# Kernel optimization log

Hardware: AMD Instinct MI355X
Metric: run time of the kernel (lower is better)

## Reference

```python
import jax, jax.numpy as jnp
import numpy as np

# db4 decomposition filters (as in get_wavelet_filters('db4'))
_H0 = jnp.array([0.0322231, -0.01260397, -0.09921954, 0.2978578,
                 0.80373875, 0.49761867, -0.02963553, -0.07576571], dtype=jnp.float32)
_H1 = jnp.array([0.07576571, -0.02963553, -0.49761867, 0.80373875,
                 -0.2978578, -0.09921954, 0.01260397, 0.0322231], dtype=jnp.float32)
LEVEL = 2
IN_CH, OUT_CH, MODES = 64, 64, 32


def subband_conv2d(x, k2d, stride):
    # depthwise (grouped) conv: same 2D filter applied per channel, NHWC
    C = x.shape[-1]
    k = jnp.tile(k2d[:, :, None, None], (1, 1, 1, C)).astype(x.dtype)  # HWIO, I=1
    return jax.lax.conv_general_dilated(
        x, k, (stride, stride), 'SAME',
        dimension_numbers=('NHWC', 'HWIO', 'NHWC'), feature_group_count=C)


def upsample2d(t):
    B, H, W, C = t.shape
    return jnp.zeros((B, 2 * H, 2 * W, C), t.dtype).at[:, ::2, ::2, :].set(t)


def setup_inputs() -> dict:
    key = jax.random.key(0)
    kx, k1, k2, k3, k4 = jax.random.split(key, 5)
    scale = 1.0 / (IN_CH * OUT_CH)
    wshape = (IN_CH, OUT_CH, MODES, MODES)
    return {
        'x': jax.random.normal(kx, (32, 128, 128, IN_CH), dtype=jnp.float32),
        'weights1': scale * jax.random.uniform(k1, wshape, dtype=jnp.float32),
        'weights2': scale * jax.random.uniform(k2, wshape, dtype=jnp.float32),
        'weights3': scale * jax.random.uniform(k3, wshape, dtype=jnp.float32),
        'weights4': scale * jax.random.uniform(k4, wshape, dtype=jnp.float32),
    }


def reference(x, weights1, weights2, weights3, weights4):
    # H=W=128 == size and divisible by 2**LEVEL: pad branch and effective_level
    # adjustment in the original are no-ops.
    h0, h1 = _H0, _H1
    g0, g1 = h0[::-1], h1[::-1]  # reconstruction filters

    # ---- multi-level 2D DWT (depthwise strided convs per subband) ----
    approx = x
    details = []
    for _ in range(LEVEL):
        lh = subband_conv2d(approx, jnp.outer(h0, h1), 2)
        hl = subband_conv2d(approx, jnp.outer(h1, h0), 2)
        hh = subband_conv2d(approx, jnp.outer(h1, h1), 2)
        approx = subband_conv2d(approx, jnp.outer(h0, h0), 2)
        details.append((lh, hl, hh))

    # ---- per-pixel channel mixing on final LL and last-level details ----
    ah, aw = approx.shape[1], approx.shape[2]
    out_ft = jnp.einsum('bhwi,iohw->bhwo', approx, weights1[:, :, :ah, :aw])
    last_lh, last_hl, last_hh = details[-1]
    dh, dw = last_lh.shape[1], last_lh.shape[2]
    out_lh = jnp.einsum('bhwi,iohw->bhwo', last_lh, weights2[:, :, :dh, :dw])
    out_hl = jnp.einsum('bhwi,iohw->bhwo', last_hl, weights3[:, :, :dh, :dw])
    out_hh = jnp.einsum('bhwi,iohw->bhwo', last_hh, weights4[:, :, :dh, :dw])

    # ---- IDWT reconstruction ----
    # Deepest level: all four subbands contribute. Earlier levels: details are
    # zeroed in the original, and conv(zeros)=0, so only the LL path remains.
    res = (subband_conv2d(upsample2d(out_ft), jnp.outer(g0, g0), 1)
           + subband_conv2d(upsample2d(out_lh), jnp.outer(g0, g1), 1)
           + subband_conv2d(upsample2d(out_hl), jnp.outer(g1, g0), 1)
           + subband_conv2d(upsample2d(out_hh), jnp.outer(g1, g1), 1))
    for _ in range(LEVEL - 1):
        res = subband_conv2d(upsample2d(res), jnp.outer(g0, g0), 1)
    return res
```

## Files before the change

### kernel.cpp

```cpp
#include <hip/hip_runtime.h>


__constant__ float c_h0[8] = {0.0322231f, -0.01260397f, -0.09921954f, 0.2978578f,
                              0.80373875f, 0.49761867f, -0.02963553f, -0.07576571f};
__constant__ float c_h1[8] = {0.07576571f, -0.02963553f, -0.49761867f, 0.80373875f,
                              -0.2978578f, -0.09921954f, 0.01260397f, 0.0322231f};
__constant__ float c_g0[8] = {-0.07576571f, -0.02963553f, 0.49761867f, 0.80373875f,
                              0.2978578f, -0.09921954f, -0.01260397f, 0.0322231f};
__constant__ float c_g1[8] = {0.0322231f, 0.01260397f, -0.09921954f, -0.2978578f,
                              0.80373875f, -0.49761867f, -0.02963553f, 0.07576571f};

__device__ __forceinline__ float4 f4z() { return make_float4(0.f, 0.f, 0.f, 0.f); }
__device__ __forceinline__ float4 f4fma(float4 a, float w, float4 v) {
  a.x = fmaf(w, v.x, a.x); a.y = fmaf(w, v.y, a.y);
  a.z = fmaf(w, v.z, a.z); a.w = fmaf(w, v.w, a.w);
  return a;
}

__global__ __launch_bounds__(256) void k_dwt1t(const float* __restrict__ x,
                                               float* __restrict__ ll1,
                                               const float* __restrict__ w1,
                                               const float* __restrict__ w2,
                                               const float* __restrict__ w3,
                                               const float* __restrict__ w4,
                                               float* __restrict__ wt) {
  __shared__ float4 sRow[2][40 * 17];
  int t = threadIdx.x;
  int bid = blockIdx.x;

  if (bid >= 1024) {
    int bid2 = bid - 1024;
    int s   = bid2 >> 12;
    int rem = bid2 & 4095;
    int hw0 = (rem & 31) * 32;
    int io0 = (rem >> 5) * 32;
    const float* w = (s == 0) ? w1 : (s == 1) ? w2 : (s == 2) ? w3 : w4;
    float* tile = (float*)sRow;
    int tx = t & 31;
    int ty = t >> 5;
#pragma unroll
    for (int k = 0; k < 4; ++k) {
      int r = ty + k * 8;
      tile[r * 33 + tx] = w[(io0 + r) * 1024 + hw0 + tx];
    }
    __syncthreads();
    float* o = wt + (size_t)s * 4194304;
#pragma unroll
    for (int k = 0; k < 4; ++k) {
      int r = ty + k * 8;
      o[(hw0 + r) * 4096 + io0 + tx] = tile[tx * 33 + r];
    }
    return;
  }

  int c4 = t & 15;
  int owl = t >> 4;
  int owb = bid & 3;
  int ohc = (bid >> 2) & 7;
  int b   = bid >> 5;
  int ow0 = owb * 16;
  int ow  = ow0 + owl;
  int oh0 = ohc * 8;
  int iw_start = 2 * ow0 - 3;
  const float* xb = x + ((size_t)b << 20);

  auto stage2 = [&](int ih0) {
#pragma unroll
    for (int base = 0; base < 80; base += 16) {
      int item = base + owl;
      int rw   = item >= 40 ? 1 : 0;
      int iw_s = item - rw * 40;
      int ihc  = min(max(ih0 + rw, 0), 127);
      int iwc  = min(max(iw_start + iw_s, 0), 127);
      sRow[rw][iw_s * 17 + c4] =
          *(const float4*)(xb + (size_t)ihc * 8192 + (iwc << 6) + (c4 << 2));
    }
  };

  auto hrowL = [&](int rw, int ih) -> float4 {
    float4 r = f4z();
    if ((unsigned)ih >= 128u) return r;
#pragma unroll
    for (int j = 0; j < 8; ++j) {
      int iw  = 2 * ow - 3 + j;
      int iwc = min(max(iw, 0), 127);
      int iw_s = iwc - iw_start;
      float w = ((unsigned)iw < 128u) ? c_h0[j] : 0.f;
      r = f4fma(r, w, sRow[rw][iw_s * 17 + c4]);
    }
    return r;
  };

  float4 ring[8];
  int ihb = 2 * oh0 - 3;
#pragma unroll
  for (int pk = 0; pk < 3; ++pk) {
    stage2(ihb + 2 * pk);
    __syncthreads();
    ring[2 * pk]     = hrowL(0, ihb + 2 * pk);
    ring[2 * pk + 1] = hrowL(1, ihb + 2 * pk + 1);
    __syncthreads();
  }
  float* outp = ll1 + ((((size_t)b * 64 + oh0) * 64 + ow) << 6) + (c4 << 2);
#pragma unroll
  for (int oo = 0; oo < 8; ++oo) {
    stage2(ihb + 6);
    __syncthreads();
    ring[6] = hrowL(0, ihb + 6);
    ring[7] = hrowL(1, ihb + 7);
    float4 a = f4z();
#pragma unroll
    for (int i = 0; i < 8; ++i) a = f4fma(a, c_h0[i], ring[i]);
    *(float4*)(outp + oo * 4096) = a;
    __syncthreads();
#pragma unroll
    for (int k = 0; k < 6; ++k) ring[k] = ring[k + 2];
    ihb += 2;
  }
}

__global__ __launch_bounds__(256) void k_dwt2(const float* __restrict__ ll1,
                                              float* __restrict__ subs) {
  __shared__ float4 sRow[2][40 * 17];
  int t = threadIdx.x;
  int c4 = t & 15;
  int owl = t >> 4;
  int bid = blockIdx.x;
  int owb = bid & 1;
  int ohc = (bid >> 1) & 7;
  int b   = bid >> 4;
  int ow0 = owb * 16;
  int ow  = ow0 + owl;
  int oh0 = ohc * 4;
  int iw_start = 2 * ow0 - 3;
  const float* lb = ll1 + ((size_t)b << 18);

  auto stage2 = [&](int ih0) {
#pragma unroll
    for (int base = 0; base < 80; base += 16) {
      int item = base + owl;
      int rw   = item >= 40 ? 1 : 0;
      int iw_s = item - rw * 40;
      int ihc  = min(max(ih0 + rw, 0), 63);
      int iwc  = min(max(iw_start + iw_s, 0), 63);
      sRow[rw][iw_s * 17 + c4] =
          *(const float4*)(lb + (size_t)ihc * 4096 + (iwc << 6) + (c4 << 2));
    }
  };

  auto hrow2L = [&](int rw, int ih, float4& rl, float4& rh) {
    rl = f4z(); rh = f4z();
    if ((unsigned)ih >= 64u) return;
#pragma unroll
    for (int j = 0; j < 8; ++j) {
      int iw  = 2 * ow - 3 + j;
      int iwc = min(max(iw, 0), 63);
      int iw_s = iwc - iw_start;
      bool ok = (unsigned)iw < 64u;
      float wl = ok ? c_h0[j] : 0.f;
      float wh = ok ? c_h1[j] : 0.f;
      float4 v = sRow[rw][iw_s * 17 + c4];
      rl = f4fma(rl, wl, v);
      rh = f4fma(rh, wh, v);
    }
  };

  float4 Rl[8], Rh[8];
  int ihb = 2 * oh0 - 3;
#pragma unroll
  for (int pk = 0; pk < 3; ++pk) {
    stage2(ihb + 2 * pk);
    __syncthreads();
    hrow2L(0, ihb + 2 * pk,     Rl[2 * pk],     Rh[2 * pk]);
    hrow2L(1, ihb + 2 * pk + 1, Rl[2 * pk + 1], Rh[2 * pk + 1]);
    __syncthreads();
  }
  float* outp = subs + ((((size_t)b * 32 + oh0) * 32 + ow) << 6) + (c4 << 2);
#pragma unroll
  for (int oo = 0; oo < 4; ++oo) {
    stage2(ihb + 6);
    __syncthreads();
    hrow2L(0, ihb + 6, Rl[6], Rh[6]);
    hrow2L(1, ihb + 7, Rl[7], Rh[7]);
    float4 a_ll = f4z(), a_lh = f4z(), a_hl = f4z(), a_hh = f4z();
#pragma unroll
    for (int i = 0; i < 8; ++i) {
      a_ll = f4fma(a_ll, c_h0[i], Rl[i]);
      a_lh = f4fma(a_lh, c_h0[i], Rh[i]);
      a_hl = f4fma(a_hl, c_h1[i], Rl[i]);
      a_hh = f4fma(a_hh, c_h1[i], Rh[i]);
    }
    float* o = outp + oo * 2048;
    *(float4*)(o)           = a_ll;
    *(float4*)(o + 2097152) = a_lh;
    *(float4*)(o + 4194304) = a_hl;
    *(float4*)(o + 6291456) = a_hh;
    __syncthreads();
#pragma unroll
    for (int k = 0; k < 6; ++k) { Rl[k] = Rl[k + 2]; Rh[k] = Rh[k + 2]; }
    ihb += 2;
  }
}

__global__ __launch_bounds__(256) void k_einsum(const float* __restrict__ subs,
                                               const float* __restrict__ w1,
                                               const float* __restrict__ w2,
                                               const float* __restrict__ w3,
                                               const float* __restrict__ w4,
                                               const float* __restrict__ wt,
                                               float* __restrict__ eout,
                                               int use_wt) {
  __shared__ float sW[4096];
  __shared__ float sA[2048];
  int p = blockIdx.x;
  int s = blockIdx.y;
  int t = threadIdx.x;
  const float* A = subs + (size_t)s * 2097152;
  if (use_wt) {
    const float* Wp = wt + (size_t)s * 4194304 + (size_t)p * 4096;
#pragma unroll
    for (int k = 0; k < 16; ++k) sW[t + 256 * k] = Wp[t + 256 * k];
  } else {
    const float* Ws = (s == 0) ? w1 : (s == 1) ? w2 : (s == 2) ? w3 : w4;
#pragma unroll
    for (int k = 0; k < 16; ++k) {
      int e = t + 256 * k;
      sW[e] = Ws[e * 1024 + p];
    }
  }
#pragma unroll
  for (int k = 0; k < 8; ++k) {
    int e = t + 256 * k;
    sA[e] = A[(e >> 6) * 65536 + (p << 6) + (e & 63)];
  }
  __syncthreads();
  int o  = t & 63;
  int bg = t >> 6;
  float acc[8] = {0.f, 0.f, 0.f, 0.f, 0.f, 0.f, 0.f, 0.f};
  for (int i = 0; i < 64; ++i) {
    float wv = sW[(i << 6) + o];
#pragma unroll
    for (int k = 0; k < 8; ++k) acc[k] += sA[((bg * 8 + k) << 6) + i] * wv;
  }
  float* Oo = eout + (size_t)s * 2097152 + (p << 6) + o;
#pragma unroll
  for (int k = 0; k < 8; ++k) Oo[(bg * 8 + k) * 65536] = acc[k];
}

__global__ __launch_bounds__(256) void k_invfinal(const float* __restrict__ eout,
                                                  float* __restrict__ out) {
  __shared__ float4 sRes[3][2][20][16];
  int t = threadIdx.x;
  int c4 = t & 15;
  int ql = t >> 4;
  int bid = blockIdx.x;
  int xt = bid & 3;
  int yt = (bid >> 2) & 3;
  int b  = bid >> 4;
  int q0 = xt * 16;
  int qi0 = (q0 >> 1) - 1;
  int qi = qi0 + ql;
  int r0p = yt * 8;

  auto loadrowI = [&](int m, float4& ae, float4& ao, float4& be, float4& bo) {
    ae = f4z(); ao = f4z(); be = f4z(); bo = f4z();
    if ((unsigned)m >= 32u) return;
    const float* base = eout + ((((size_t)b * 32 + m) * 32) << 6) + (c4 << 2);
    float4 vf[4], vl[4], vh[4], vv[4];
#pragma unroll
    for (int dn = -1; dn <= 2; ++dn) {
      int n = qi + dn;
      int nc = min(max(n, 0), 31);
      const float* p = base + (nc << 6);
      vf[dn + 1] = *(const float4*)(p);
      vl[dn + 1] = *(const float4*)(p + 2097152);
      vh[dn + 1] = *(const float4*)(p + 4194304);
      vv[dn + 1] = *(const float4*)(p + 6291456);
    }
#pragma unroll
    for (int dn = -1; dn <= 2; ++dn) {
      int n = qi + dn;
      bool ok = (unsigned)n < 32u;
      float g0e = ok ? c_g0[2 * dn + 3] : 0.f, g1e = ok ? c_g1[2 * dn + 3] : 0.f;
      float g0o = ok ? c_g0[2 * dn + 2] : 0.f, g1o = ok ? c_g1[2 * dn + 2] : 0.f;
      ae = f4fma(ae, g0e, vf[dn + 1]); ae = f4fma(ae, g1e, vl[dn + 1]);
      ao = f4fma(ao, g0o, vf[dn + 1]); ao = f4fma(ao, g1o, vl[dn + 1]);
      be = f4fma(be, g0e, vh[dn + 1]); be = f4fma(be, g1e, vv[dn + 1]);
      bo = f4fma(bo, g0o, vh[dn + 1]); bo = f4fma(bo, g1o, vv[dn + 1]);
    }
  };

  float4 Ae[4], Ao[4], Be[4], Bo[4];
  int prs = r0p - 1;

  auto steppair = [&]() {
    loadrowI(prs + 2, Ae[3], Ao[3], Be[3], Bo[3]);
    float4 ee = f4z(), eo = f4z(), oe = f4z(), oo = f4z();
    if ((unsigned)prs < 32u) {
#pragma unroll
      for (int dm = 0; dm < 4; ++dm) {
        float gye = c_g0[2 * dm + 1], hye = c_g1[2 * dm + 1];
        float gyo = c_g0[2 * dm],     hyo = c_g1[2 * dm];
        ee = f4fma(ee, gye, Ae[dm]); ee = f4fma(ee, hye, Be[dm]);
        eo = f4fma(eo, gye, Ao[dm]); eo = f4fma(eo, hye, Bo[dm]);
        oe = f4fma(oe, gyo, Ae[dm]); oe = f4fma(oe, hyo, Be[dm]);
        oo = f4fma(oo, gyo, Ao[dm]); oo = f4fma(oo, hyo, Bo[dm]);
      }
    }
    int slot = ((prs % 3) + 3) % 3;
    sRes[slot][0][2 * ql][c4]     = ee;
    sRes[slot][0][2 * ql + 1][c4] = eo;
    sRes[slot][1][2 * ql][c4]     = oe;
    sRes[slot][1][2 * ql + 1][c4] = oo;
#pragma unroll
    for (int k = 0; k < 3; ++k) {
      Ae[k] = Ae[k + 1]; Ao[k] = Ao[k + 1]; Be[k] = Be[k + 1]; Bo[k] = Bo[k + 1];
    }
  };

  if (ql < 10) {
    loadrowI(prs - 1, Ae[0], Ao[0], Be[0], Bo[0]);
    loadrowI(prs,     Ae[1], Ao[1], Be[1], Bo[1]);
    loadrowI(prs + 1, Ae[2], Ao[2], Be[2], Bo[2]);
  }
#pragma unroll
  for (int pk = 0; pk < 2; ++pk) {
    if (ql < 10) steppair();
    ++prs;
  }
  int q = q0 + ql;
#pragma unroll
  for (int it = 0; it < 8; ++it) {
    if (ql < 10) steppair();
    __syncthreads();
    float4 H0[5], H1[5];
#pragma unroll
    for (int mi = 0; mi < 5; ++mi) {
      int m = 2 * (prs - 1) - 1 + mi;
      int pm = m >> 1;
      int ey = m & 1;
      int slot = ((pm % 3) + 3) % 3;
      float4 h0v = f4z(), h1v = f4z();
#pragma unroll
      for (int dn = -1; dn <= 2; ++dn) {
        int n = q + dn;
        bool ok = (unsigned)n < 64u;
        float we = ok ? c_g0[2 * dn + 3] : 0.f;
        float wo = ok ? c_g0[2 * dn + 2] : 0.f;
        float4 v = sRes[slot][ey][ql + 2 + dn][c4];
        h0v = f4fma(h0v, we, v);
        h1v = f4fma(h1v, wo, v);
      }
      H0[mi] = h0v; H1[mi] = h1v;
    }
#pragma unroll
    for (int rr2 = 0; rr2 < 2; ++rr2) {
      int r = 2 * (prs - 1) + rr2;
      float4 aee = f4z(), aeo = f4z(), aoe = f4z(), aoo = f4z();
#pragma unroll
      for (int dm = 0; dm < 4; ++dm) {
        float gye = c_g0[2 * dm + 1];
        float gyo = c_g0[2 * dm];
        aee = f4fma(aee, gye, H0[rr2 + dm]);
        aeo = f4fma(aeo, gye, H1[rr2 + dm]);
        aoe = f4fma(aoe, gyo, H0[rr2 + dm]);
        aoo = f4fma(aoo, gyo, H1[rr2 + dm]);
      }
      int y = 2 * r, xx = 2 * q;
      float* ob = out + (((size_t)(b * 128 + y)) * 128 + xx) * 64 + (c4 << 2);
      *(float4*)(ob)              = aee;
      *(float4*)(ob + 64)         = aeo;
      *(float4*)(ob + 8192)       = aoe;
      *(float4*)(ob + 8192 + 64)  = aoo;
    }
    __syncthreads();
    ++prs;
  }
}

extern "C" void kernel_launch(void* const* d_in, const int* in_sizes, int n_in,
                              void* d_out, int out_size, void* d_ws, size_t ws_size,
                              hipStream_t stream) {
  (void)in_sizes; (void)n_in; (void)out_size;
  const float* x  = (const float*)d_in[0];
  const float* w1 = (const float*)d_in[1];
  const float* w2 = (const float*)d_in[2];
  const float* w3 = (const float*)d_in[3];
  const float* w4 = (const float*)d_in[4];
  float* out = (float*)d_out;
  float* ws  = (float*)d_ws;

  float* ll1  = ws;
  float* subs = ws + 8388608;
  float* eout = ws + 16777216;
  float* wt   = ws + 25165824;
  int use_wt = (ws_size >= (size_t)41943040 * 4) ? 1 : 0;

  int g1 = use_wt ? (1024 + 16384) : 1024;
  k_dwt1t<<<g1, 256, 0, stream>>>(x, ll1, w1, w2, w3, w4, wt);
  k_dwt2<<<512, 256, 0, stream>>>(ll1, subs);
  k_einsum<<<dim3(1024, 4), 256, 0, stream>>>(subs, w1, w2, w3, w4, wt, eout, use_wt);
  k_invfinal<<<512, 256, 0, stream>>>(eout, out);
}
```

Before: 372.8 us.

## Enlarge first-level DWT row tiles and widen weight-transpose tiles with float4

```diff
diff --git a/kernel.cpp b/kernel.cpp
--- a/kernel.cpp
+++ b/kernel.cpp
@@ -24,31 +24,40 @@
                                                const float* __restrict__ w3,
                                                const float* __restrict__ w4,
                                                float* __restrict__ wt) {
-  __shared__ float4 sRow[2][40 * 17];
+  __shared__ float4 sRow[4][40 * 17];
   int t = threadIdx.x;
   int bid = blockIdx.x;
 
-  if (bid >= 1024) {
-    int bid2 = bid - 1024;
-    int s   = bid2 >> 12;
-    int rem = bid2 & 4095;
-    int hw0 = (rem & 31) * 32;
-    int io0 = (rem >> 5) * 32;
+  if (bid >= 512) {
+    int bid2 = bid - 512;
+    int s   = bid2 >> 10;
+    int rem = bid2 & 1023;
+    int hw0 = (rem & 15) << 6;
+    int io0 = (rem >> 4) << 6;
     const float* w = (s == 0) ? w1 : (s == 1) ? w2 : (s == 2) ? w3 : w4;
     float* tile = (float*)sRow;
-    int tx = t & 31;
-    int ty = t >> 5;
+    int c = t & 15;
+    int r = t >> 4;
 #pragma unroll
     for (int k = 0; k < 4; ++k) {
-      int r = ty + k * 8;
-      tile[r * 33 + tx] = w[(io0 + r) * 1024 + hw0 + tx];
+      int io = r + 16 * k;
+      float4 v = *(const float4*)(w + (size_t)(io0 + io) * 1024 + hw0 + c * 4);
+      tile[io * 65 + c * 4 + 0] = v.x;
+      tile[io * 65 + c * 4 + 1] = v.y;
+      tile[io * 65 + c * 4 + 2] = v.z;
+      tile[io * 65 + c * 4 + 3] = v.w;
     }
     __syncthreads();
     float* o = wt + (size_t)s * 4194304;
 #pragma unroll
     for (int k = 0; k < 4; ++k) {
-      int r = ty + k * 8;
-      o[(hw0 + r) * 4096 + io0 + tx] = tile[tx * 33 + r];
+      int hr = r + 16 * k;
+      float4 v;
+      v.x = tile[(c * 4 + 0) * 65 + hr];
+      v.y = tile[(c * 4 + 1) * 65 + hr];
+      v.z = tile[(c * 4 + 2) * 65 + hr];
+      v.w = tile[(c * 4 + 3) * 65 + hr];
+      *(float4*)(o + (size_t)(hw0 + hr) * 4096 + io0 + c * 4) = v;
     }
     return;
   }
@@ -56,19 +65,19 @@
   int c4 = t & 15;
   int owl = t >> 4;
   int owb = bid & 3;
-  int ohc = (bid >> 2) & 7;
-  int b   = bid >> 5;
+  int ohc = (bid >> 2) & 3;
+  int b   = bid >> 4;
   int ow0 = owb * 16;
   int ow  = ow0 + owl;
-  int oh0 = ohc * 8;
+  int oh0 = ohc * 16;
   int iw_start = 2 * ow0 - 3;
   const float* xb = x + ((size_t)b << 20);
 
-  auto stage2 = [&](int ih0) {
-#pragma unroll
-    for (int base = 0; base < 80; base += 16) {
+  auto stageN = [&](int ih0, int nrows) {
+    int items = nrows * 40;
+    for (int base = 0; base < items; base += 16) {
       int item = base + owl;
-      int rw   = item >= 40 ? 1 : 0;
+      int rw   = item / 40;
       int iw_s = item - rw * 40;
       int ihc  = min(max(ih0 + rw, 0), 127);
       int iwc  = min(max(iw_start + iw_s, 0), 127);
@@ -91,31 +100,41 @@
     return r;
   };
 
-  float4 ring[8];
+  float4 ring[10];
   int ihb = 2 * oh0 - 3;
-#pragma unroll
-  for (int pk = 0; pk < 3; ++pk) {
-    stage2(ihb + 2 * pk);
-    __syncthreads();
-    ring[2 * pk]     = hrowL(0, ihb + 2 * pk);
-    ring[2 * pk + 1] = hrowL(1, ihb + 2 * pk + 1);
-    __syncthreads();
-  }
+  stageN(ihb, 4);
+  __syncthreads();
+#pragma unroll
+  for (int k = 0; k < 4; ++k) ring[k] = hrowL(k, ihb + k);
+  __syncthreads();
+  stageN(ihb + 4, 4);
+  __syncthreads();
+#pragma unroll
+  for (int k = 0; k < 4; ++k) ring[4 + k] = hrowL(k, ihb + 4 + k);
+  __syncthreads();
+
   float* outp = ll1 + ((((size_t)b * 64 + oh0) * 64 + ow) << 6) + (c4 << 2);
 #pragma unroll
-  for (int oo = 0; oo < 8; ++oo) {
-    stage2(ihb + 6);
-    __syncthreads();
-    ring[6] = hrowL(0, ihb + 6);
-    ring[7] = hrowL(1, ihb + 7);
-    float4 a = f4z();
-#pragma unroll
-    for (int i = 0; i < 8; ++i) a = f4fma(a, c_h0[i], ring[i]);
-    *(float4*)(outp + oo * 4096) = a;
-    __syncthreads();
-#pragma unroll
-    for (int k = 0; k < 6; ++k) ring[k] = ring[k + 2];
-    ihb += 2;
+  for (int p = 0; p < 8; ++p) {
+    int nfill = (p == 0) ? 2 : 4;
+    int fill0 = 10 - nfill;
+    stageN(ihb + 4 * p + fill0, nfill);
+    __syncthreads();
+#pragma unroll
+    for (int k = 0; k < 4; ++k) {
+      if (k < nfill) ring[fill0 + k] = hrowL(k, ihb + 4 * p + fill0 + k);
+    }
+    float4 a0 = f4z(), a1 = f4z();
+#pragma unroll
+    for (int i = 0; i < 8; ++i) {
+      a0 = f4fma(a0, c_h0[i], ring[i]);
+      a1 = f4fma(a1, c_h0[i], ring[i + 2]);
+    }
+    *(float4*)(outp + (2 * p) * 4096)     = a0;
+    *(float4*)(outp + (2 * p + 1) * 4096) = a1;
+    __syncthreads();
+#pragma unroll
+    for (int k = 0; k < 6; ++k) ring[k] = ring[k + 4];
   }
 }
 
@@ -396,7 +415,7 @@
   float* wt   = ws + 25165824;
   int use_wt = (ws_size >= (size_t)41943040 * 4) ? 1 : 0;
 
-  int g1 = use_wt ? (1024 + 16384) : 1024;
+  int g1 = use_wt ? (512 + 4096) : 512;
   k_dwt1t<<<g1, 256, 0, stream>>>(x, ll1, w1, w2, w3, w4, wt);
   k_dwt2<<<512, 256, 0, stream>>>(ll1, subs);
   k_einsum<<<dim3(1024, 4), 256, 0, stream>>>(subs, w1, w2, w3, w4, wt, eout, use_wt);
```

After: 364.9 us. -2.1%, faster.
